# Kernel tuning notes

Measured on AMD Instinct MI355X. Metric: run time of the kernel, lower is better.

## Reference

```python
import jax, jax.numpy as jnp
import numpy as np

N_NODES = 100000
N_REL = 8
N_EDGES = 1_600_000
ED = 64   # entity_dim
RD = 64   # relation_dim
H = 4     # attention heads
A = 16    # attention dim per head
D1, D2 = 32, 16  # conv_dim_list


def _leaky(x):
    return jax.nn.leaky_relu(x, 0.01)  # nn.LeakyReLU default slope


def _l2norm(x):
    n = jnp.sqrt(jnp.sum(x * x, axis=1, keepdims=True))
    return x / jnp.maximum(n, 1e-12)  # F.normalize(p=2, dim=1)


def setup_inputs() -> dict:
    key = jax.random.key(0)
    ks = jax.random.split(key, 16)
    s = 0.1
    return dict(
        src=jax.random.randint(ks[0], (N_EDGES,), 0, N_NODES),
        dst=jax.random.randint(ks[1], (N_EDGES,), 0, N_NODES),
        etype=jax.random.randint(ks[2], (N_EDGES,), 0, N_REL),
        node_ids=jnp.arange(N_NODES),
        user_ids=jax.random.randint(ks[3], (1000,), 0, N_NODES),
        item_ids=jax.random.randint(ks[4], (4096,), 0, N_NODES),
        entity_embed=jax.random.normal(ks[5], (N_NODES, ED)) * s,
        rel_embed=jax.random.normal(ks[6], (N_REL, RD)) * s,
        W_R=jax.random.normal(ks[7], (N_REL, ED, RD)) * s,
        W_A=jax.random.normal(ks[8], (RD, H, A)) * s,
        W1_0=jax.random.normal(ks[9], (ED, D1 // H)) * s,
        b1_0=jnp.zeros((D1 // H,)),
        W2_0=jax.random.normal(ks[10], (ED, D1 // H)) * s,
        b2_0=jnp.zeros((D1 // H,)),
        W1_1=jax.random.normal(ks[11], (D1, D2 // H)) * s,
        b1_1=jnp.zeros((D2 // H,)),
        W2_1=jax.random.normal(ks[12], (D1, D2 // H)) * s,
        b2_1=jnp.zeros((D2 // H,)),
    )


def _compute_attention(entity_embed, rel_embed, W_R, W_A, src, dst, etype):
    # relation-specific edge attention: tanh(e_src W_r W_A) * tanh(e_dst W_r W_A + r W_A)
    WA_flat = W_A.reshape(RD, H * A)
    W_ra = jnp.einsum('rij,jk->rik', W_R, WA_flat)          # [R, ED, H*A]
    proj = jnp.einsum('ne,rek->rnk', entity_embed, W_ra)    # [R, N, H*A]
    r_emb_a = rel_embed @ WA_flat                           # [R, H*A]
    r_mul_t = jnp.tanh(proj[etype, src])                    # [E, H*A]
    r_mul_h = jnp.tanh(proj[etype, dst] + r_emb_a[etype])   # [E, H*A]
    att = (r_mul_t * r_mul_h).reshape(-1, H, A).sum(-1)     # [E, H]
    # edge softmax over incoming edges of each dst node, per head
    m = jax.ops.segment_max(att, dst, num_segments=N_NODES)
    m = jnp.where(jnp.isfinite(m), m, 0.0)
    e = jnp.exp(att - m[dst])
    z = jax.ops.segment_sum(e, dst, num_segments=N_NODES)
    return e / jnp.maximum(z[dst], 1e-12)                   # [E, H]


def _bi_layer(ego, att, src, dst, W1, b1, W2, b2, out_dim):
    # u_mul_e + sum: message = node[src] (broadcast over heads) * att[:, :, None]
    in_dim = ego.shape[1]
    msg = ego[src][:, None, :] * att[:, :, None]            # [E, H, in]
    N_h = jax.ops.segment_sum(msg, dst, num_segments=N_NODES)  # [N, H, in]
    node = ego[:, None, :]                                  # [N, 1, in]
    out1 = _leaky((node + N_h).reshape(-1, in_dim) @ W1 + b1).reshape(N_NODES, out_dim)
    out2 = _leaky((node * N_h).reshape(-1, in_dim) @ W2 + b2).reshape(N_NODES, out_dim)
    return out1 + out2  # dropout p=0 (eval)


def reference(src, dst, etype, node_ids, user_ids, item_ids,
              entity_embed, rel_embed, W_R, W_A,
              W1_0, b1_0, W2_0, b2_0, W1_1, b1_1, W2_1, b2_1):
    att = _compute_attention(entity_embed, rel_embed, W_R, W_A, src, dst, etype)
    ego = entity_embed[node_ids]
    ego1 = _bi_layer(ego, att, src, dst, W1_0, b1_0, W2_0, b2_0, D1)
    ego2 = _bi_layer(ego1, att, src, dst, W1_1, b1_1, W2_1, b2_1, D2)
    all_embed = jnp.concatenate([ego, _l2norm(ego1), _l2norm(ego2)], axis=1)  # [N, 112]
    return all_embed[user_ids] @ all_embed[item_ids].T     # [1000, 4096]
```

## Files before the change

### kernel.cpp

```cpp
#include <hip/hip_runtime.h>
#include <hip/hip_bf16.h>
#include <math.h>

#define NN 100000
#define NR 8
#define NE 1600000

typedef __attribute__((ext_vector_type(8))) short short8v;
typedef __attribute__((ext_vector_type(4))) float float4v;
typedef __attribute__((ext_vector_type(2))) float float2v;

__device__ inline float bf2f(unsigned short u) {
  union { unsigned int i; float f; } v; v.i = ((unsigned int)u) << 16; return v.f;
}
__device__ inline unsigned short f2bf(float f) {
  __hip_bfloat16 h = __float2bfloat16(f);
  return *reinterpret_cast<unsigned short*>(&h);
}
__device__ inline float fast_tanh(float x) {
  float ex = __expf(2.f * x);
  return 1.f - 2.f * __builtin_amdgcn_rcpf(ex + 1.f);
}

__global__ void k_prep(const float* __restrict__ W_R, const float* __restrict__ W_A,
                       const float* __restrict__ rel, unsigned short* __restrict__ Wbf,
                       float* __restrict__ r_emb_a) {
  int tid = blockIdx.x * 256 + threadIdx.x;
  if (tid < NR * 64 * 64) {
    int r = tid >> 12;
    int i = (tid >> 6) & 63;
    int k = tid & 63;
    float acc = 0.f;
    const float* wr = W_R + (r * 64 + i) * 64;
    for (int j = 0; j < 64; ++j) acc += wr[j] * W_A[j * 64 + k];
    Wbf[(r * 64 + k) * 64 + i] = f2bf(acc);
  } else if (tid < NR * 64 * 64 + NR * 64) {
    int idx = tid - NR * 64 * 64;
    int r = idx >> 6, k = idx & 63;
    float acc = 0.f;
    for (int j = 0; j < 64; ++j) acc += rel[r * 64 + j] * W_A[j * 64 + k];
    r_emb_a[idx] = acc;
  }
}

__global__ void k_cvt(const float* __restrict__ E, unsigned short* __restrict__ Ebf) {
  int i = blockIdx.x * 256 + threadIdx.x;
  float4 v = ((const float4*)E)[i];
  ushort4 o;
  o.x = f2bf(v.x); o.y = f2bf(v.y); o.z = f2bf(v.z); o.w = f2bf(v.w);
  ((ushort4*)Ebf)[i] = o;
}

__global__ void k_proj(const unsigned short* __restrict__ Ebf,
                       const unsigned short* __restrict__ Wbf,
                       const float* __restrict__ rea,
                       unsigned char* __restrict__ T1n, unsigned char* __restrict__ T2n) {
  int wv = threadIdx.x >> 6, lane = threadIdx.x & 63;
  int n0 = blockIdx.x * 64 + wv * 16;
  int mrow = lane & 15, kg = lane >> 4;
  int node = n0 + mrow;
  int nodeC = (node < NN) ? node : NN - 1;
  bool ok = (node < NN);
  const short8v b0 = *(const short8v*)(Ebf + (long)nodeC * 64 + kg * 8);
  const short8v b1 = *(const short8v*)(Ebf + (long)nodeC * 64 + 32 + kg * 8);
  for (int ct = 0; ct < 32; ++ct) {
    int ca = ct * 16 + mrow;
    const short8v a0 = *(const short8v*)(Wbf + ca * 64 + kg * 8);
    const short8v a1 = *(const short8v*)(Wbf + ca * 64 + 32 + kg * 8);
    float4v acc = {0.f, 0.f, 0.f, 0.f};
    acc = __builtin_amdgcn_mfma_f32_16x16x32_bf16(a0, b0, acc, 0, 0, 0);
    acc = __builtin_amdgcn_mfma_f32_16x16x32_bf16(a1, b1, acc, 0, 0, 0);
    int c0 = ct * 16 + kg * 4;
    float4 rv4 = *(const float4*)(rea + c0);
    unsigned int p1 = __builtin_amdgcn_cvt_pk_fp8_f32(fast_tanh(acc[0]), fast_tanh(acc[1]), 0u, false);
    p1 = __builtin_amdgcn_cvt_pk_fp8_f32(fast_tanh(acc[2]), fast_tanh(acc[3]), p1, true);
    unsigned int p2 = __builtin_amdgcn_cvt_pk_fp8_f32(fast_tanh(acc[0] + rv4.x), fast_tanh(acc[1] + rv4.y), 0u, false);
    p2 = __builtin_amdgcn_cvt_pk_fp8_f32(fast_tanh(acc[2] + rv4.z), fast_tanh(acc[3] + rv4.w), p2, true);
    if (ok) {
      *(unsigned int*)(T1n + (long)node * 512 + c0) = p1;
      *(unsigned int*)(T2n + (long)node * 512 + c0) = p2;
    }
  }
}

__global__ void k_hist(const int* __restrict__ dst, int* __restrict__ cnt) {
  int e = blockIdx.x * 256 + threadIdx.x;
  if (e < NE) atomicAdd(&cnt[dst[e]], 1);
}

#define SCAN_B 1024
#define NSCAN ((NN + SCAN_B - 1) / SCAN_B)

__global__ void k_scan1(const int* __restrict__ cnt, int* __restrict__ rowp,
                        int* __restrict__ bsum) {
  __shared__ int s[SCAN_B];
  int t = threadIdx.x, g = blockIdx.x * SCAN_B + t;
  s[t] = (g < NN) ? cnt[g] : 0;
  __syncthreads();
  for (int off = 1; off < SCAN_B; off <<= 1) {
    int x = (t >= off) ? s[t - off] : 0;
    __syncthreads();
    s[t] += x;
    __syncthreads();
  }
  if (g < NN) rowp[g + 1] = s[t];
  if (t == SCAN_B - 1) bsum[blockIdx.x] = s[t];
}

__global__ void k_scan2(int* bsum) {
  if (threadIdx.x == 0) {
    int acc = 0;
    for (int i = 0; i < NSCAN; ++i) { int v = bsum[i]; bsum[i] = acc; acc += v; }
  }
}

__global__ void k_scan3(int* rowp, const int* __restrict__ bsum) {
  int t = threadIdx.x, g = blockIdx.x * SCAN_B + t;
  if (g < NN) rowp[g + 1] += bsum[blockIdx.x];
  if (g == 0) rowp[0] = 0;
}

__global__ void k_scatter(const int* __restrict__ src, const int* __restrict__ dst,
                          const int* __restrict__ etype, const int* __restrict__ rowp,
                          int* __restrict__ cur, uint2* __restrict__ rec) {
  int e = blockIdx.x * 256 + threadIdx.x;
  if (e >= NE) return;
  int d = dst[e];
  int p = rowp[d] + atomicAdd(&cur[d], 1);
  uint2 rv;
  rv.x = ((unsigned int)src[e] << 3) | (unsigned int)etype[e];
  rv.y = (unsigned int)d;
  rec[p] = rv;
}

__global__ void k_fused0(const float* __restrict__ E, const unsigned short* __restrict__ Ebf,
                         const unsigned char* __restrict__ T1n,
                         const unsigned char* __restrict__ T2n,
                         const uint2* __restrict__ rec, const int* __restrict__ rowp,
                         float* __restrict__ att4, float* __restrict__ zinv4,
                         const float* __restrict__ W1, const float* __restrict__ b1,
                         const float* __restrict__ W2, const float* __restrict__ b2,
                         float* __restrict__ ego1, unsigned short* __restrict__ ego1bf) {
  __shared__ float wt1[8][68], wt2[8][68];
  __shared__ float bb[16];
  __shared__ float s1[4][4][68], s2[4][4][68];
  int t = threadIdx.x;
  for (int i = t; i < 512; i += 256) {
    int d = i >> 3, j = i & 7;
    wt1[j][d] = W1[i];
    wt2[j][d] = W2[i];
  }
  if (t < 8) bb[t] = b1[t];
  else if (t < 16) bb[t] = b2[t - 8];
  __syncthreads();
  int wv = t >> 6, lane = t & 63;
  int n = blockIdx.x * 4 + wv;
  int p0 = rowp[n], p1 = rowp[n + 1];
  int g = lane >> 4, q = lane & 15;
  int bl = (lane & 48) | (lane & 3);
  const unsigned int* recw = (const unsigned int*)rec;
  float acc[4][4];
#pragma unroll
  for (int h = 0; h < 4; ++h)
#pragma unroll
    for (int j = 0; j < 4; ++j) acc[h][j] = 0.f;
  float z0 = 0.f, z1 = 0.f, z2 = 0.f, z3 = 0.f;
  for (int p = p0 + g; p < p1; p += 4) {
    unsigned int rv = recw[p * 2];
    int s = (int)(rv >> 3), r = (int)(rv & 7);
    unsigned int aw = *(const unsigned int*)(T1n + (long)s * 512 + r * 64 + q * 4);
    unsigned int bw = *(const unsigned int*)(T2n + (long)n * 512 + r * 64 + q * 4);
    float2v fa0 = __builtin_amdgcn_cvt_pk_f32_fp8(aw, false);
    float2v fa1 = __builtin_amdgcn_cvt_pk_f32_fp8(aw, true);
    float2v fb0 = __builtin_amdgcn_cvt_pk_f32_fp8(bw, false);
    float2v fb1 = __builtin_amdgcn_cvt_pk_f32_fp8(bw, true);
    float dot = fa0.x * fb0.x + fa0.y * fb0.y + fa1.x * fb1.x + fa1.y * fb1.y;
    dot += __shfl_xor(dot, 1);
    dot += __shfl_xor(dot, 2);
    float e = __expf(dot);
    float e0 = __shfl(e, bl);
    float e1 = __shfl(e, bl + 4);
    float e2 = __shfl(e, bl + 8);
    float e3 = __shfl(e, bl + 12);
    z0 += e0; z1 += e1; z2 += e2; z3 += e3;
    if (q == 0) ((float4*)att4)[p] = make_float4(e0, e1, e2, e3);
    ushort4 ev = *(const ushort4*)(Ebf + s * 64 + q * 4);
    float v0 = bf2f(ev.x), v1 = bf2f(ev.y), v2 = bf2f(ev.z), v3 = bf2f(ev.w);
    acc[0][0] += e0 * v0; acc[0][1] += e0 * v1; acc[0][2] += e0 * v2; acc[0][3] += e0 * v3;
    acc[1][0] += e1 * v0; acc[1][1] += e1 * v1; acc[1][2] += e1 * v2; acc[1][3] += e1 * v3;
    acc[2][0] += e2 * v0; acc[2][1] += e2 * v1; acc[2][2] += e2 * v2; acc[2][3] += e2 * v3;
    acc[3][0] += e3 * v0; acc[3][1] += e3 * v1; acc[3][2] += e3 * v2; acc[3][3] += e3 * v3;
  }
#pragma unroll
  for (int h = 0; h < 4; ++h)
#pragma unroll
    for (int j = 0; j < 4; ++j) {
      acc[h][j] += __shfl_xor(acc[h][j], 16);
      acc[h][j] += __shfl_xor(acc[h][j], 32);
    }
  z0 += __shfl_xor(z0, 16); z0 += __shfl_xor(z0, 32);
  z1 += __shfl_xor(z1, 16); z1 += __shfl_xor(z1, 32);
  z2 += __shfl_xor(z2, 16); z2 += __shfl_xor(z2, 32);
  z3 += __shfl_xor(z3, 16); z3 += __shfl_xor(z3, 32);
  float zi0 = 1.f / fmaxf(z0, 1e-12f);
  float zi1 = 1.f / fmaxf(z1, 1e-12f);
  float zi2 = 1.f / fmaxf(z2, 1e-12f);
  float zi3 = 1.f / fmaxf(z3, 1e-12f);
  if (lane == 0) *(float4*)(zinv4 + n * 4) = make_float4(zi0, zi1, zi2, zi3);
  if (lane < 16) {
    acc[0][0] *= zi0; acc[0][1] *= zi0; acc[0][2] *= zi0; acc[0][3] *= zi0;
    acc[1][0] *= zi1; acc[1][1] *= zi1; acc[1][2] *= zi1; acc[1][3] *= zi1;
    acc[2][0] *= zi2; acc[2][1] *= zi2; acc[2][2] *= zi2; acc[2][3] *= zi2;
    acc[3][0] *= zi3; acc[3][1] *= zi3; acc[3][2] *= zi3; acc[3][3] *= zi3;
    float4 edv = *(const float4*)(E + n * 64 + q * 4);
#pragma unroll
    for (int h = 0; h < 4; ++h) {
      float4 v1v, v2v;
      v1v.x = edv.x + acc[h][0]; v2v.x = edv.x * acc[h][0];
      v1v.y = edv.y + acc[h][1]; v2v.y = edv.y * acc[h][1];
      v1v.z = edv.z + acc[h][2]; v2v.z = edv.z * acc[h][2];
      v1v.w = edv.w + acc[h][3]; v2v.w = edv.w * acc[h][3];
      *(float4*)&s1[wv][h][q * 4] = v1v;
      *(float4*)&s2[wv][h][q * 4] = v2v;
    }
  }
  __syncthreads();
  int h = (lane >> 3) & 3, j = lane & 7;
  const float* sp = (lane < 32) ? &s1[wv][h][0] : &s2[wv][h][0];
  const float* wp = (lane < 32) ? &wt1[j][0] : &wt2[j][0];
  float o = 0.f;
#pragma unroll
  for (int d = 0; d < 64; d += 4) {
    float4 sv = *(const float4*)(sp + d);
    float4 wv4 = *(const float4*)(wp + d);
    o += sv.x * wv4.x + sv.y * wv4.y + sv.z * wv4.z + sv.w * wv4.w;
  }
  o += (lane < 32) ? bb[j] : bb[8 + j];
  o = (o >= 0.f) ? o : 0.01f * o;
  float other = __shfl_xor(o, 32);
  if (lane < 32) {
    float r = o + other;
    ego1[n * 32 + h * 8 + j] = r;
    ego1bf[n * 32 + h * 8 + j] = f2bf(r);
  }
}

__global__ void k_fused1(const float* __restrict__ ego1, const unsigned short* __restrict__ E1bf,
                         const float* __restrict__ att4, const float* __restrict__ zinv4,
                         const uint2* __restrict__ rec, const int* __restrict__ rowp,
                         const float* __restrict__ W1, const float* __restrict__ b1,
                         const float* __restrict__ W2, const float* __restrict__ b2,
                         float* __restrict__ ego2) {
  __shared__ float wt1[4][36], wt2[4][36], bb[8];
  __shared__ float s1[4][4][36], s2[4][4][36];
  int t = threadIdx.x;
  if (t < 128) { int d = t >> 2, j = t & 3; wt1[j][d] = W1[t]; wt2[j][d] = W2[t]; }
  if (t < 4) bb[t] = b1[t];
  else if (t < 8) bb[t] = b2[t - 4];
  __syncthreads();
  int wv = t >> 6, lane = t & 63;
  int n = blockIdx.x * 4 + wv;
  int p0 = rowp[n], p1 = rowp[n + 1];
  int g = lane >> 3, q = lane & 7;
  const unsigned int* recw = (const unsigned int*)rec;
  float acc[4][4];
#pragma unroll
  for (int h = 0; h < 4; ++h)
#pragma unroll
    for (int j = 0; j < 4; ++j) acc[h][j] = 0.f;
  for (int p = p0 + g; p < p1; p += 8) {
    int s = (int)(recw[p * 2] >> 3);
    float4 a = ((const float4*)att4)[p];
    ushort4 ev = *(const ushort4*)(E1bf + s * 32 + q * 4);
    float e0 = bf2f(ev.x), e1 = bf2f(ev.y), e2 = bf2f(ev.z), e3 = bf2f(ev.w);
    acc[0][0] += a.x * e0; acc[0][1] += a.x * e1; acc[0][2] += a.x * e2; acc[0][3] += a.x * e3;
    acc[1][0] += a.y * e0; acc[1][1] += a.y * e1; acc[1][2] += a.y * e2; acc[1][3] += a.y * e3;
    acc[2][0] += a.z * e0; acc[2][1] += a.z * e1; acc[2][2] += a.z * e2; acc[2][3] += a.z * e3;
    acc[3][0] += a.w * e0; acc[3][1] += a.w * e1; acc[3][2] += a.w * e2; acc[3][3] += a.w * e3;
  }
#pragma unroll
  for (int h = 0; h < 4; ++h)
#pragma unroll
    for (int j = 0; j < 4; ++j) {
      acc[h][j] += __shfl_xor(acc[h][j], 8);
      acc[h][j] += __shfl_xor(acc[h][j], 16);
      acc[h][j] += __shfl_xor(acc[h][j], 32);
    }
  if (lane < 8) {
    float4 zi = *(const float4*)(zinv4 + n * 4);
#pragma unroll
    for (int j = 0; j < 4; ++j) {
      acc[0][j] *= zi.x; acc[1][j] *= zi.y; acc[2][j] *= zi.z; acc[3][j] *= zi.w;
    }
    float4 e1v = *(const float4*)(ego1 + n * 32 + q * 4);
#pragma unroll
    for (int h = 0; h < 4; ++h) {
      float4 v1, v2;
      v1.x = e1v.x + acc[h][0]; v2.x = e1v.x * acc[h][0];
      v1.y = e1v.y + acc[h][1]; v2.y = e1v.y * acc[h][1];
      v1.z = e1v.z + acc[h][2]; v2.z = e1v.z * acc[h][2];
      v1.w = e1v.w + acc[h][3]; v2.w = e1v.w * acc[h][3];
      *(float4*)&s1[wv][h][q * 4] = v1;
      *(float4*)&s2[wv][h][q * 4] = v2;
    }
  }
  __syncthreads();
  if (lane < 32) {
    int h = (lane >> 2) & 3, j = lane & 3;
    const float* sp = (lane < 16) ? &s1[wv][h][0] : &s2[wv][h][0];
    const float* wp = (lane < 16) ? &wt1[j][0] : &wt2[j][0];
    float o = 0.f;
#pragma unroll
    for (int dd = 0; dd < 32; dd += 4) {
      float4 sv = *(const float4*)(sp + dd);
      float4 wv4 = *(const float4*)(wp + dd);
      o += sv.x * wv4.x + sv.y * wv4.y + sv.z * wv4.z + sv.w * wv4.w;
    }
    o += (lane < 16) ? bb[j] : bb[4 + j];
    o = (o >= 0.f) ? o : 0.01f * o;
    float other = __shfl_xor(o, 16);
    if (lane < 16) ego2[n * 16 + h * 4 + j] = o + other;
  }
}

__global__ void k_uv(const float* __restrict__ E, const float* __restrict__ E1,
                     const float* __restrict__ E2, const int* __restrict__ uid,
                     const int* __restrict__ iid, float* __restrict__ U,
                     float* __restrict__ V) {
  int row = (blockIdx.x * 256 + threadIdx.x) >> 6;
  int lane = threadIdx.x & 63;
  if (row >= 1000 + 4096) return;
  int id = (row < 1000) ? uid[row] : iid[row - 1000];
  float* dest = (row < 1000) ? (U + row * 112) : (V + (row - 1000) * 112);
  float v1 = (lane < 32) ? E1[id * 32 + lane] : 0.f;
  float s1 = v1 * v1;
  for (int m = 1; m < 64; m <<= 1) s1 += __shfl_xor(s1, m);
  float v2 = (lane < 16) ? E2[id * 16 + lane] : 0.f;
  float s2 = v2 * v2;
  for (int m = 1; m < 64; m <<= 1) s2 += __shfl_xor(s2, m);
  float i1 = 1.f / fmaxf(sqrtf(s1), 1e-12f);
  float i2 = 1.f / fmaxf(sqrtf(s2), 1e-12f);
  dest[lane] = E[id * 64 + lane];
  if (lane < 32) dest[64 + lane] = v1 * i1;
  if (lane < 16) dest[96 + lane] = v2 * i2;
}

__global__ void k_gemm(const float* __restrict__ U, const float* __restrict__ V,
                       float* __restrict__ C) {
  __shared__ float Us[16][113], Vs[16][113];
  int tx = threadIdx.x & 15, ty = threadIdx.x >> 4;
  int u0 = blockIdx.y * 16, v0 = blockIdx.x * 16;
  for (int i = threadIdx.x; i < 16 * 112; i += 256) {
    int rr = i / 112, cc = i % 112;
    int ur = u0 + rr;
    Us[rr][cc] = (ur < 1000) ? U[ur * 112 + cc] : 0.f;
    Vs[rr][cc] = V[(v0 + rr) * 112 + cc];
  }
  __syncthreads();
  int u = u0 + ty;
  if (u >= 1000) return;
  float acc = 0.f;
#pragma unroll
  for (int k = 0; k < 112; ++k) acc += Us[ty][k] * Vs[tx][k];
  C[u * 4096 + v0 + tx] = acc;
}

extern "C" void kernel_launch(void* const* d_in, const int* in_sizes, int n_in,
                              void* d_out, int out_size, void* d_ws, size_t ws_size,
                              hipStream_t stream) {
  const int* src = (const int*)d_in[0];
  const int* dst = (const int*)d_in[1];
  const int* etype = (const int*)d_in[2];
  const int* uid = (const int*)d_in[4];
  const int* iid = (const int*)d_in[5];
  const float* entity = (const float*)d_in[6];
  const float* rel = (const float*)d_in[7];
  const float* W_R = (const float*)d_in[8];
  const float* W_A = (const float*)d_in[9];
  const float* W1_0 = (const float*)d_in[10];
  const float* b1_0 = (const float*)d_in[11];
  const float* W2_0 = (const float*)d_in[12];
  const float* b2_0 = (const float*)d_in[13];
  const float* W1_1 = (const float*)d_in[14];
  const float* b1_1 = (const float*)d_in[15];
  const float* W2_1 = (const float*)d_in[16];
  const float* b2_1 = (const float*)d_in[17];
  float* out = (float*)d_out;

  char* ws = (char*)d_ws;
  unsigned char*  T1n  = (unsigned char*) (ws + 0);
  unsigned char*  T2n  = (unsigned char*) (ws + 51200000);
  float*          att4 = (float*)         (ws + 102400000);
  uint2*          rec  = (uint2*)         (ws + 128000000);
  int*            rowp = (int*)           (ws + 140800000);
  int*            cnt  = (int*)           (ws + 141200128);
  int*            bsum = (int*)           (ws + 141600256);
  unsigned short* Wbf  = (unsigned short*)(ws + 141600768);
  float*          rea  = (float*)         (ws + 141666304);
  unsigned short* Ebf  = (unsigned short*)(ws + 141668352);
  float*          zinv4= (float*)         (ws + 154468352);
  float*          ego1 = (float*)         (ws + 156068352);
  unsigned short* e1bf = (unsigned short*)(ws + 168868352);
  float*          ego2 = (float*)         (ws + 175268352);
  float*          U    = (float*)         (ws + 181668352);
  float*          V    = (float*)         (ws + 182116352);

  hipMemsetAsync(cnt, 0, NN * sizeof(int), stream);
  k_prep<<<130, 256, 0, stream>>>(W_R, W_A, rel, Wbf, rea);
  k_cvt<<<6250, 256, 0, stream>>>(entity, Ebf);
  k_proj<<<(NN + 63) / 64, 256, 0, stream>>>(Ebf, Wbf, rea, T1n, T2n);
  k_hist<<<NE / 256, 256, 0, stream>>>(dst, cnt);
  k_scan1<<<NSCAN, SCAN_B, 0, stream>>>(cnt, rowp, bsum);
  k_scan2<<<1, 64, 0, stream>>>(bsum);
  k_scan3<<<NSCAN, SCAN_B, 0, stream>>>(rowp, bsum);
  hipMemsetAsync(cnt, 0, NN * sizeof(int), stream);
  k_scatter<<<NE / 256, 256, 0, stream>>>(src, dst, etype, rowp, cnt, rec);
  k_fused0<<<NN / 4, 256, 0, stream>>>(entity, Ebf, T1n, T2n, rec, rowp,
                                       att4, zinv4, W1_0, b1_0, W2_0, b2_0,
                                       ego1, e1bf);
  k_fused1<<<NN / 4, 256, 0, stream>>>(ego1, e1bf, att4, zinv4, rec, rowp,
                                       W1_1, b1_1, W2_1, b2_1, ego2);
  k_uv<<<(1000 + 4096 + 3) / 4, 256, 0, stream>>>(entity, ego1, ego2, uid, iid, U, V);
  k_gemm<<<dim3(4096 / 16, (1000 + 15) / 16), 256, 0, stream>>>(U, V, out);
}
```

Measured before the change: 581.4 us.

## Record edge slot in histogram and widen per-lane gathers to 8 elements

The histogram kernel now stores each edge's atomic slot, so the scatter pass reuses it instead of clearing the counters and doing a second atomic pass. In both aggregation kernels each lane now loads 8 values per gather (64-bit fp8 and 128-bit bf16 loads), so each wave processes twice as many edges per iteration. This aims to cut atomic traffic and issue more bytes per memory instruction. In exchange it adds an extra 6.4 MB epos array, doubles accumulator registers, and adds one more shuffle-reduction stage.

```diff
diff --git a/kernel.cpp b/kernel.cpp
--- a/kernel.cpp
+++ b/kernel.cpp
@@ -83,9 +83,10 @@
   }
 }
 
-__global__ void k_hist(const int* __restrict__ dst, int* __restrict__ cnt) {
+__global__ void k_hist(const int* __restrict__ dst, int* __restrict__ cnt,
+                       int* __restrict__ epos) {
   int e = blockIdx.x * 256 + threadIdx.x;
-  if (e < NE) atomicAdd(&cnt[dst[e]], 1);
+  if (e < NE) epos[e] = atomicAdd(&cnt[dst[e]], 1);
 }
 
 #define SCAN_B 1024
@@ -122,11 +123,11 @@
 
 __global__ void k_scatter(const int* __restrict__ src, const int* __restrict__ dst,
                           const int* __restrict__ etype, const int* __restrict__ rowp,
-                          int* __restrict__ cur, uint2* __restrict__ rec) {
+                          const int* __restrict__ epos, uint2* __restrict__ rec) {
   int e = blockIdx.x * 256 + threadIdx.x;
   if (e >= NE) return;
   int d = dst[e];
-  int p = rowp[d] + atomicAdd(&cur[d], 1);
+  int p = rowp[d] + epos[e];
   uint2 rv;
   rv.x = ((unsigned int)src[e] << 3) | (unsigned int)etype[e];
   rv.y = (unsigned int)d;
@@ -156,72 +157,88 @@
   int wv = t >> 6, lane = t & 63;
   int n = blockIdx.x * 4 + wv;
   int p0 = rowp[n], p1 = rowp[n + 1];
-  int g = lane >> 4, q = lane & 15;
-  int bl = (lane & 48) | (lane & 3);
+  int g = lane >> 3, q = lane & 7;
+  int gbase = lane & 56;
   const unsigned int* recw = (const unsigned int*)rec;
-  float acc[4][4];
+  float acc[4][8];
 #pragma unroll
   for (int h = 0; h < 4; ++h)
 #pragma unroll
-    for (int j = 0; j < 4; ++j) acc[h][j] = 0.f;
+    for (int j = 0; j < 8; ++j) acc[h][j] = 0.f;
   float z0 = 0.f, z1 = 0.f, z2 = 0.f, z3 = 0.f;
-  for (int p = p0 + g; p < p1; p += 4) {
+  for (int p = p0 + g; p < p1; p += 8) {
     unsigned int rv = recw[p * 2];
     int s = (int)(rv >> 3), r = (int)(rv & 7);
-    unsigned int aw = *(const unsigned int*)(T1n + (long)s * 512 + r * 64 + q * 4);
-    unsigned int bw = *(const unsigned int*)(T2n + (long)n * 512 + r * 64 + q * 4);
-    float2v fa0 = __builtin_amdgcn_cvt_pk_f32_fp8(aw, false);
-    float2v fa1 = __builtin_amdgcn_cvt_pk_f32_fp8(aw, true);
-    float2v fb0 = __builtin_amdgcn_cvt_pk_f32_fp8(bw, false);
-    float2v fb1 = __builtin_amdgcn_cvt_pk_f32_fp8(bw, true);
-    float dot = fa0.x * fb0.x + fa0.y * fb0.y + fa1.x * fb1.x + fa1.y * fb1.y;
+    uint2 aw = *(const uint2*)(T1n + (long)s * 512 + r * 64 + q * 8);
+    uint2 bw = *(const uint2*)(T2n + (long)n * 512 + r * 64 + q * 8);
+    float2v a0 = __builtin_amdgcn_cvt_pk_f32_fp8(aw.x, false);
+    float2v a1 = __builtin_amdgcn_cvt_pk_f32_fp8(aw.x, true);
+    float2v a2 = __builtin_amdgcn_cvt_pk_f32_fp8(aw.y, false);
+    float2v a3 = __builtin_amdgcn_cvt_pk_f32_fp8(aw.y, true);
+    float2v c0 = __builtin_amdgcn_cvt_pk_f32_fp8(bw.x, false);
+    float2v c1 = __builtin_amdgcn_cvt_pk_f32_fp8(bw.x, true);
+    float2v c2 = __builtin_amdgcn_cvt_pk_f32_fp8(bw.y, false);
+    float2v c3 = __builtin_amdgcn_cvt_pk_f32_fp8(bw.y, true);
+    float dot = a0.x * c0.x + a0.y * c0.y + a1.x * c1.x + a1.y * c1.y
+              + a2.x * c2.x + a2.y * c2.y + a3.x * c3.x + a3.y * c3.y;
     dot += __shfl_xor(dot, 1);
-    dot += __shfl_xor(dot, 2);
     float e = __expf(dot);
-    float e0 = __shfl(e, bl);
-    float e1 = __shfl(e, bl + 4);
-    float e2 = __shfl(e, bl + 8);
-    float e3 = __shfl(e, bl + 12);
+    float e0 = __shfl(e, gbase + 0);
+    float e1 = __shfl(e, gbase + 2);
+    float e2 = __shfl(e, gbase + 4);
+    float e3 = __shfl(e, gbase + 6);
     z0 += e0; z1 += e1; z2 += e2; z3 += e3;
     if (q == 0) ((float4*)att4)[p] = make_float4(e0, e1, e2, e3);
-    ushort4 ev = *(const ushort4*)(Ebf + s * 64 + q * 4);
-    float v0 = bf2f(ev.x), v1 = bf2f(ev.y), v2 = bf2f(ev.z), v3 = bf2f(ev.w);
-    acc[0][0] += e0 * v0; acc[0][1] += e0 * v1; acc[0][2] += e0 * v2; acc[0][3] += e0 * v3;
-    acc[1][0] += e1 * v0; acc[1][1] += e1 * v1; acc[1][2] += e1 * v2; acc[1][3] += e1 * v3;
-    acc[2][0] += e2 * v0; acc[2][1] += e2 * v1; acc[2][2] += e2 * v2; acc[2][3] += e2 * v3;
-    acc[3][0] += e3 * v0; acc[3][1] += e3 * v1; acc[3][2] += e3 * v2; acc[3][3] += e3 * v3;
+    short8v ev8 = *(const short8v*)(Ebf + (long)s * 64 + q * 8);
+#pragma unroll
+    for (int j = 0; j < 8; ++j) {
+      float v = bf2f((unsigned short)ev8[j]);
+      acc[0][j] += e0 * v;
+      acc[1][j] += e1 * v;
+      acc[2][j] += e2 * v;
+      acc[3][j] += e3 * v;
+    }
   }
 #pragma unroll
   for (int h = 0; h < 4; ++h)
 #pragma unroll
-    for (int j = 0; j < 4; ++j) {
+    for (int j = 0; j < 8; ++j) {
+      acc[h][j] += __shfl_xor(acc[h][j], 8);
       acc[h][j] += __shfl_xor(acc[h][j], 16);
       acc[h][j] += __shfl_xor(acc[h][j], 32);
     }
-  z0 += __shfl_xor(z0, 16); z0 += __shfl_xor(z0, 32);
-  z1 += __shfl_xor(z1, 16); z1 += __shfl_xor(z1, 32);
-  z2 += __shfl_xor(z2, 16); z2 += __shfl_xor(z2, 32);
-  z3 += __shfl_xor(z3, 16); z3 += __shfl_xor(z3, 32);
+  z0 += __shfl_xor(z0, 8); z0 += __shfl_xor(z0, 16); z0 += __shfl_xor(z0, 32);
+  z1 += __shfl_xor(z1, 8); z1 += __shfl_xor(z1, 16); z1 += __shfl_xor(z1, 32);
+  z2 += __shfl_xor(z2, 8); z2 += __shfl_xor(z2, 16); z2 += __shfl_xor(z2, 32);
+  z3 += __shfl_xor(z3, 8); z3 += __shfl_xor(z3, 16); z3 += __shfl_xor(z3, 32);
   float zi0 = 1.f / fmaxf(z0, 1e-12f);
   float zi1 = 1.f / fmaxf(z1, 1e-12f);
   float zi2 = 1.f / fmaxf(z2, 1e-12f);
   float zi3 = 1.f / fmaxf(z3, 1e-12f);
   if (lane == 0) *(float4*)(zinv4 + n * 4) = make_float4(zi0, zi1, zi2, zi3);
-  if (lane < 16) {
-    acc[0][0] *= zi0; acc[0][1] *= zi0; acc[0][2] *= zi0; acc[0][3] *= zi0;
-    acc[1][0] *= zi1; acc[1][1] *= zi1; acc[1][2] *= zi1; acc[1][3] *= zi1;
-    acc[2][0] *= zi2; acc[2][1] *= zi2; acc[2][2] *= zi2; acc[2][3] *= zi2;
-    acc[3][0] *= zi3; acc[3][1] *= zi3; acc[3][2] *= zi3; acc[3][3] *= zi3;
-    float4 edv = *(const float4*)(E + n * 64 + q * 4);
+  if (lane < 8) {
+    float zi[4] = {zi0, zi1, zi2, zi3};
+    float4 eda = *(const float4*)(E + n * 64 + q * 8);
+    float4 edb = *(const float4*)(E + n * 64 + q * 8 + 4);
 #pragma unroll
     for (int h = 0; h < 4; ++h) {
-      float4 v1v, v2v;
-      v1v.x = edv.x + acc[h][0]; v2v.x = edv.x * acc[h][0];
-      v1v.y = edv.y + acc[h][1]; v2v.y = edv.y * acc[h][1];
-      v1v.z = edv.z + acc[h][2]; v2v.z = edv.z * acc[h][2];
-      v1v.w = edv.w + acc[h][3]; v2v.w = edv.w * acc[h][3];
-      *(float4*)&s1[wv][h][q * 4] = v1v;
-      *(float4*)&s2[wv][h][q * 4] = v2v;
+      float4 v1a, v2a, v1b, v2b;
+      float m0 = acc[h][0] * zi[h], m1 = acc[h][1] * zi[h];
+      float m2 = acc[h][2] * zi[h], m3 = acc[h][3] * zi[h];
+      float m4 = acc[h][4] * zi[h], m5 = acc[h][5] * zi[h];
+      float m6 = acc[h][6] * zi[h], m7 = acc[h][7] * zi[h];
+      v1a.x = eda.x + m0; v2a.x = eda.x * m0;
+      v1a.y = eda.y + m1; v2a.y = eda.y * m1;
+      v1a.z = eda.z + m2; v2a.z = eda.z * m2;
+      v1a.w = eda.w + m3; v2a.w = eda.w * m3;
+      v1b.x = edb.x + m4; v2b.x = edb.x * m4;
+      v1b.y = edb.y + m5; v2b.y = edb.y * m5;
+      v1b.z = edb.z + m6; v2b.z = edb.z * m6;
+      v1b.w = edb.w + m7; v2b.w = edb.w * m7;
+      *(float4*)&s1[wv][h][q * 8] = v1a;
+      *(float4*)&s1[wv][h][q * 8 + 4] = v1b;
+      *(float4*)&s2[wv][h][q * 8] = v2a;
+      *(float4*)&s2[wv][h][q * 8 + 4] = v2b;
     }
   }
   __syncthreads();
@@ -261,47 +278,59 @@
   int wv = t >> 6, lane = t & 63;
   int n = blockIdx.x * 4 + wv;
   int p0 = rowp[n], p1 = rowp[n + 1];
-  int g = lane >> 3, q = lane & 7;
+  int g = lane >> 2, q = lane & 3;
   const unsigned int* recw = (const unsigned int*)rec;
-  float acc[4][4];
+  float acc[4][8];
 #pragma unroll
   for (int h = 0; h < 4; ++h)
 #pragma unroll
-    for (int j = 0; j < 4; ++j) acc[h][j] = 0.f;
-  for (int p = p0 + g; p < p1; p += 8) {
+    for (int j = 0; j < 8; ++j) acc[h][j] = 0.f;
+  for (int p = p0 + g; p < p1; p += 16) {
     int s = (int)(recw[p * 2] >> 3);
     float4 a = ((const float4*)att4)[p];
-    ushort4 ev = *(const ushort4*)(E1bf + s * 32 + q * 4);
-    float e0 = bf2f(ev.x), e1 = bf2f(ev.y), e2 = bf2f(ev.z), e3 = bf2f(ev.w);
-    acc[0][0] += a.x * e0; acc[0][1] += a.x * e1; acc[0][2] += a.x * e2; acc[0][3] += a.x * e3;
-    acc[1][0] += a.y * e0; acc[1][1] += a.y * e1; acc[1][2] += a.y * e2; acc[1][3] += a.y * e3;
-    acc[2][0] += a.z * e0; acc[2][1] += a.z * e1; acc[2][2] += a.z * e2; acc[2][3] += a.z * e3;
-    acc[3][0] += a.w * e0; acc[3][1] += a.w * e1; acc[3][2] += a.w * e2; acc[3][3] += a.w * e3;
+    short8v ev8 = *(const short8v*)(E1bf + (long)s * 32 + q * 8);
+#pragma unroll
+    for (int j = 0; j < 8; ++j) {
+      float v = bf2f((unsigned short)ev8[j]);
+      acc[0][j] += a.x * v;
+      acc[1][j] += a.y * v;
+      acc[2][j] += a.z * v;
+      acc[3][j] += a.w * v;
+    }
   }
 #pragma unroll
   for (int h = 0; h < 4; ++h)
 #pragma unroll
-    for (int j = 0; j < 4; ++j) {
+    for (int j = 0; j < 8; ++j) {
+      acc[h][j] += __shfl_xor(acc[h][j], 4);
       acc[h][j] += __shfl_xor(acc[h][j], 8);
       acc[h][j] += __shfl_xor(acc[h][j], 16);
       acc[h][j] += __shfl_xor(acc[h][j], 32);
     }
-  if (lane < 8) {
+  if (lane < 4) {
     float4 zi = *(const float4*)(zinv4 + n * 4);
-#pragma unroll
-    for (int j = 0; j < 4; ++j) {
-      acc[0][j] *= zi.x; acc[1][j] *= zi.y; acc[2][j] *= zi.z; acc[3][j] *= zi.w;
-    }
-    float4 e1v = *(const float4*)(ego1 + n * 32 + q * 4);
+    float zih[4] = {zi.x, zi.y, zi.z, zi.w};
+    float4 e1a = *(const float4*)(ego1 + n * 32 + q * 8);
+    float4 e1b = *(const float4*)(ego1 + n * 32 + q * 8 + 4);
 #pragma unroll
     for (int h = 0; h < 4; ++h) {
-      float4 v1, v2;
-      v1.x = e1v.x + acc[h][0]; v2.x = e1v.x * acc[h][0];
-      v1.y = e1v.y + acc[h][1]; v2.y = e1v.y * acc[h][1];
-      v1.z = e1v.z + acc[h][2]; v2.z = e1v.z * acc[h][2];
-      v1.w = e1v.w + acc[h][3]; v2.w = e1v.w * acc[h][3];
-      *(float4*)&s1[wv][h][q * 4] = v1;
-      *(float4*)&s2[wv][h][q * 4] = v2;
+      float m0 = acc[h][0] * zih[h], m1 = acc[h][1] * zih[h];
+      float m2 = acc[h][2] * zih[h], m3 = acc[h][3] * zih[h];
+      float m4 = acc[h][4] * zih[h], m5 = acc[h][5] * zih[h];
+      float m6 = acc[h][6] * zih[h], m7 = acc[h][7] * zih[h];
+      float4 v1a, v2a, v1b, v2b;
+      v1a.x = e1a.x + m0; v2a.x = e1a.x * m0;
+      v1a.y = e1a.y + m1; v2a.y = e1a.y * m1;
+      v1a.z = e1a.z + m2; v2a.z = e1a.z * m2;
+      v1a.w = e1a.w + m3; v2a.w = e1a.w * m3;
+      v1b.x = e1b.x + m4; v2b.x = e1b.x * m4;
+      v1b.y = e1b.y + m5; v2b.y = e1b.y * m5;
+      v1b.z = e1b.z + m6; v2b.z = e1b.z * m6;
+      v1b.w = e1b.w + m7; v2b.w = e1b.w * m7;
+      *(float4*)&s1[wv][h][q * 8] = v1a;
+      *(float4*)&s1[wv][h][q * 8 + 4] = v1b;
+      *(float4*)&s2[wv][h][q * 8] = v2a;
+      *(float4*)&s2[wv][h][q * 8 + 4] = v2b;
     }
   }
   __syncthreads();
@@ -404,17 +433,17 @@
   float*          ego2 = (float*)         (ws + 175268352);
   float*          U    = (float*)         (ws + 181668352);
   float*          V    = (float*)         (ws + 182116352);
+  int*            epos = (int*)           (ws + 183951360);
 
   hipMemsetAsync(cnt, 0, NN * sizeof(int), stream);
   k_prep<<<130, 256, 0, stream>>>(W_R, W_A, rel, Wbf, rea);
   k_cvt<<<6250, 256, 0, stream>>>(entity, Ebf);
   k_proj<<<(NN + 63) / 64, 256, 0, stream>>>(Ebf, Wbf, rea, T1n, T2n);
-  k_hist<<<NE / 256, 256, 0, stream>>>(dst, cnt);
+  k_hist<<<NE / 256, 256, 0, stream>>>(dst, cnt, epos);
   k_scan1<<<NSCAN, SCAN_B, 0, stream>>>(cnt, rowp, bsum);
   k_scan2<<<1, 64, 0, stream>>>(bsum);
   k_scan3<<<NSCAN, SCAN_B, 0, stream>>>(rowp, bsum);
-  hipMemsetAsync(cnt, 0, NN * sizeof(int), stream);
-  k_scatter<<<NE / 256, 256, 0, stream>>>(src, dst, etype, rowp, cnt, rec);
+  k_scatter<<<NE / 256, 256, 0, stream>>>(src, dst, etype, rowp, epos, rec);
   k_fused0<<<NN / 4, 256, 0, stream>>>(entity, Ebf, T1n, T2n, rec, rowp,
                                        att4, zinv4, W1_0, b1_0, W2_0, b2_0,
                                        ego1, e1bf);
```

Measured after the change: 644.8 us. 1.11x slower.
